# Kernel optimization log

Measured on AMD Instinct MI355X. Metric: run time of the kernel, lower is better.

Reference implementation:

```python
import jax, jax.numpy as jnp
import numpy as np

BN_EPS = 1e-5
EPS_GIN = 0.0  # pyg GINConv default eps

N_NODES = 50000
N_EDGES = 800000
D_IN = 128
D_OUT = 128


def setup_inputs() -> dict:
    key = jax.random.key(0)
    ks = jax.random.split(key, 6)
    x = jax.random.normal(ks[0], (N_NODES, D_IN), dtype=jnp.float32)
    edge_index = jax.random.randint(ks[1], (2, N_EDGES), 0, N_NODES, dtype=jnp.int32)
    # glorot-ish scale for the two Linear layers
    s1 = 1.0 / np.sqrt(D_IN)
    s2 = 1.0 / np.sqrt(D_OUT)
    W1 = jax.random.normal(ks[2], (D_IN, D_OUT), dtype=jnp.float32) * s1
    b1 = jnp.zeros((D_OUT,), dtype=jnp.float32)
    gamma = jnp.ones((D_OUT,), dtype=jnp.float32)
    beta = jnp.zeros((D_OUT,), dtype=jnp.float32)
    W2 = jax.random.normal(ks[3], (D_OUT, D_OUT), dtype=jnp.float32) * s2
    b2 = jnp.zeros((D_OUT,), dtype=jnp.float32)
    return {"x": x, "edge_index": edge_index, "W1": W1, "b1": b1,
            "gamma": gamma, "beta": beta, "W2": W2, "b2": b2}


def reference(x, edge_index, W1, b1, gamma, beta, W2, b2):
    n = x.shape[0]
    src, dst = edge_index[0], edge_index[1]  # source_to_target flow
    # scatter-add neighbor aggregation: agg[i] = sum_{(j->i)} x[j]
    agg = jax.ops.segment_sum(x[src], dst, num_segments=n)
    h = (1.0 + EPS_GIN) * x + agg  # GIN combine
    # Linear -> BatchNorm1d (training-mode batch stats, biased var) -> ReLU -> Linear
    h = h @ W1 + b1
    mean = jnp.mean(h, axis=0)
    var = jnp.var(h, axis=0)
    h = (h - mean) * jax.lax.rsqrt(var + BN_EPS) * gamma + beta
    h = jax.nn.relu(h)
    return h @ W2 + b2
```

## Files before the change

kernel.cpp:

```cpp
#include <hip/hip_runtime.h>
#include <hip/hip_bf16.h>

#define D 128
#define ELLW 64
#define BCAP 8192

typedef short bf16x8 __attribute__((ext_vector_type(8)));
typedef float f32x4 __attribute__((ext_vector_type(4)));

__device__ __forceinline__ ushort f32_to_bf16_rne(float f) {
    uint b = __float_as_uint(f);
    b += 0x7fffu + ((b >> 16) & 1u);
    return (ushort)(b >> 16);
}
__device__ __forceinline__ float bf16_bits_to_f32(ushort u) {
    return __uint_as_float(((uint)u) << 16);
}


__global__ __launch_bounds__(256) void prep_kernel(const float2* __restrict__ x2,
                                                   const float* __restrict__ W1,
                                                   const float* __restrict__ W2,
                                                   uint* __restrict__ xb,
                                                   ushort* __restrict__ W1T,
                                                   ushort* __restrict__ W2T,
                                                   int nhalf, int nbx) {
    int b = blockIdx.x, t = threadIdx.x;
    if (b < nbx) {
        int i = b * 256 + t;
        if (i < nhalf) {
            float2 v = x2[i];
            xb[i] = ((uint)f32_to_bf16_rne(v.y) << 16) | (uint)f32_to_bf16_rne(v.x);
        }
    } else {
        int wb = b - nbx;
        const float* W = (wb < 64) ? W1 : W2;
        ushort* WT = (wb < 64) ? W1T : W2T;
        int q = wb & 63;
        int nrow = q * 2 + (t >> 7);
        int k = t & 127;
        WT[nrow * D + k] = f32_to_bf16_rne(W[k * D + nrow]);
    }
}


__global__ __launch_bounds__(1024) void bucket_scatter_kernel(const int* __restrict__ src,
                                                              const int* __restrict__ dst,
                                                              uint* __restrict__ part,
                                                              int* __restrict__ bcnt, int m) {
    __shared__ int hist[256];
    __shared__ int cur[256];
    int t = threadIdx.x;
    if (t < 256) hist[t] = 0;
    __syncthreads();

    int base = blockIdx.x * 4096;
    uint v[4];
    int bk[4];
    bool ok[4];
#pragma unroll
    for (int j = 0; j < 4; ++j) {
        int e = base + j * 1024 + t;
        ok[j] = e < m;
        bk[j] = 0;
        if (ok[j]) {
            int s_ = src[e], d_ = dst[e];
            v[j] = ((uint)s_ << 16) | (uint)d_;
            bk[j] = d_ >> 8;
            atomicAdd(&hist[bk[j]], 1);
        }
    }
    __syncthreads();
    if (t < 256) {
        int h = hist[t];
        int g = h ? atomicAdd(&bcnt[t], h) : 0;
        cur[t] = t * BCAP + g;
    }
    __syncthreads();
#pragma unroll
    for (int j = 0; j < 4; ++j) {
        if (ok[j]) {
            int pos = atomicAdd(&cur[bk[j]], 1);
            if (pos - bk[j] * BCAP < BCAP)
                part[pos] = v[j];
        }
    }
}


__global__ __launch_bounds__(512) void bucket_ell_kernel(const uint* __restrict__ part,
                                                         const int* __restrict__ bcnt,
                                                         ushort* __restrict__ col_ell,
                                                         int* __restrict__ degv, int n) {
    __shared__ int lcur[256];
    int b = blockIdx.x, t = threadIdx.x;
    if (t < 256) lcur[t] = 0;
    __syncthreads();
    int cnt = min(bcnt[b], BCAP);
    const uint* pp = part + (size_t)b * BCAP;
    for (int i = t; i < cnt; i += 512) {
        uint v = pp[i];
        int node = (int)(v & 0xffffu);
        int r = node - (b << 8);
        int s = atomicAdd(&lcur[r], 1);
        s = min(s, ELLW - 1);
        col_ell[(size_t)node * ELLW + s] = (ushort)(v >> 16);
    }
    __syncthreads();
    int node0 = b << 8;
    if (t < 256 && node0 + t < n) degv[node0 + t] = lcur[t];
}


__global__ __launch_bounds__(256) void aggregate_kernel(const uint* __restrict__ xb,
                                                        const int* __restrict__ degv,
                                                        const ushort* __restrict__ col_ell,
                                                        uint* __restrict__ h0b, int n) {
    int node = blockIdx.x * 4 + (threadIdx.x >> 6);
    if (node >= n) return;
    int lane = threadIdx.x & 63;
    uint a = xb[node * 64 + lane];
    float sx = __uint_as_float(a << 16);
    float sy = __uint_as_float(a & 0xffff0000u);
    int deg = min(degv[node], ELLW);
    const ushort* lst = col_ell + (size_t)node * ELLW;
    int e = 0;
    for (; e + 3 < deg; e += 4) {
        int j0 = lst[e], j1 = lst[e + 1], j2 = lst[e + 2], j3 = lst[e + 3];
        uint u0 = xb[j0 * 64 + lane];
        uint u1 = xb[j1 * 64 + lane];
        uint u2 = xb[j2 * 64 + lane];
        uint u3 = xb[j3 * 64 + lane];
        sx += __uint_as_float(u0 << 16); sy += __uint_as_float(u0 & 0xffff0000u);
        sx += __uint_as_float(u1 << 16); sy += __uint_as_float(u1 & 0xffff0000u);
        sx += __uint_as_float(u2 << 16); sy += __uint_as_float(u2 & 0xffff0000u);
        sx += __uint_as_float(u3 << 16); sy += __uint_as_float(u3 & 0xffff0000u);
    }
    for (; e < deg; ++e) {
        uint u = xb[lst[e] * 64 + lane];
        sx += __uint_as_float(u << 16);
        sy += __uint_as_float(u & 0xffff0000u);
    }
    h0b[node * 64 + lane] = ((uint)f32_to_bf16_rne(sy) << 16) | (uint)f32_to_bf16_rne(sx);
}


template <bool BN_IN, bool STATS>
__global__ __launch_bounds__(256) void gemm_mfma_kernel(const ushort* __restrict__ inb,
                                                        const ushort* __restrict__ WT,
                                                        const float* __restrict__ bias,
                                                        void* __restrict__ outp,
                                                        const float* __restrict__ scale_shift,
                                                        float* __restrict__ bn_sums,
                                                        int N) {
    __shared__ __align__(16) ushort hs[64 * D];
    __shared__ __align__(16) ushort wt[D * D];
    __shared__ float ss[2 * D];
    __shared__ float bs[D];
    __shared__ float bnl[2 * D];

    int tid = threadIdx.x;
    int row0 = blockIdx.x * 64;
    if (tid < D) bs[tid] = bias[tid];
    if (BN_IN) ss[tid] = scale_shift[tid];
    if (STATS && tid < 2 * D) bnl[tid] = 0.f;
    __syncthreads();

    char* hsb = (char*)hs;
    char* wtb = (char*)wt;

#pragma unroll
    for (int it = 0; it < 8; ++it) {
        int c = it * 256 + tid;
        int wn = c >> 4, k8 = c & 15;
        bf16x8 v = *(const bf16x8*)(WT + wn * D + k8 * 8);
        *(bf16x8*)(wtb + wn * 256 + ((k8 * 16) ^ ((wn & 7) << 4))) = v;
    }
#pragma unroll
    for (int it = 0; it < 4; ++it) {
        int c = it * 256 + tid;
        int row = c >> 4, k8 = c & 15;
        int gr = row0 + row;
        bf16x8 v;
        if (gr < N) {
            v = *(const bf16x8*)(inb + (size_t)gr * D + k8 * 8);
        } else {
#pragma unroll
            for (int j = 0; j < 8; ++j) v[j] = 0;
        }
        if (BN_IN) {
#pragma unroll
            for (int j = 0; j < 8; ++j) {
                int k = k8 * 8 + j;
                float f = bf16_bits_to_f32((ushort)v[j]);
                f = fmaxf(f * ss[k] + ss[D + k], 0.f);
                v[j] = (short)f32_to_bf16_rne(f);
            }
        }
        *(bf16x8*)(hsb + row * 256 + ((k8 * 16) ^ ((row & 7) << 4))) = v;
    }
    __syncthreads();

    int w = tid >> 6, l = tid & 63;
    int lrow = l & 15, lk = l >> 4;

    f32x4 acc[8];
#pragma unroll
    for (int f = 0; f < 8; ++f) acc[f] = (f32x4){0.f, 0.f, 0.f, 0.f};

    bf16x8 afr[4];
    int arow = w * 16 + lrow;
#pragma unroll
    for (int t = 0; t < 4; ++t)
        afr[t] = *(const bf16x8*)(hsb + arow * 256 + ((t * 64 + lk * 16) ^ ((arow & 7) << 4)));

#pragma unroll
    for (int f = 0; f < 8; ++f) {
        int nc = f * 16 + lrow;
#pragma unroll
        for (int t = 0; t < 4; ++t) {
            bf16x8 bfr = *(const bf16x8*)(wtb + nc * 256 + ((t * 64 + lk * 16) ^ ((nc & 7) << 4)));
            acc[f] = __builtin_amdgcn_mfma_f32_16x16x32_bf16(afr[t], bfr, acc[f], 0, 0, 0);
        }
    }

    int rbase = row0 + w * 16 + lk * 4;
#pragma unroll
    for (int f = 0; f < 8; ++f) {
        int colc = f * 16 + lrow;
        float bv = bs[colc];
        float s = 0.f, q = 0.f;
#pragma unroll
        for (int r = 0; r < 4; ++r) {
            int gr = rbase + r;
            if (gr < N) {
                float v = acc[f][r] + bv;
                if (STATS) {
                    ((ushort*)outp)[(size_t)gr * D + colc] = f32_to_bf16_rne(v);
                    s += v;
                    q += v * v;
                } else {
                    ((float*)outp)[(size_t)gr * D + colc] = v;
                }
            }
        }
        if (STATS) {
            s += __shfl_xor(s, 16, 64);
            s += __shfl_xor(s, 32, 64);
            q += __shfl_xor(q, 16, 64);
            q += __shfl_xor(q, 32, 64);
            if (l < 16) {
                atomicAdd(&bnl[colc], s);
                atomicAdd(&bnl[D + colc], q);
            }
        }
    }
    if (STATS) {
        __syncthreads();
        if (tid < 2 * D) atomicAdd(&bn_sums[tid], bnl[tid]);
    }
}


__global__ __launch_bounds__(128) void bn_finalize_kernel(const float* __restrict__ bn_sums,
                                                          const float* __restrict__ gamma,
                                                          const float* __restrict__ beta,
                                                          float* __restrict__ scale_shift, float invn) {
    int c = threadIdx.x;
    float mean = bn_sums[c] * invn;
    float var = bn_sums[D + c] * invn - mean * mean;
    float rstd = rsqrtf(var + 1e-5f);
    float sc = gamma[c] * rstd;
    scale_shift[c] = sc;
    scale_shift[D + c] = beta[c] - mean * sc;
}


extern "C" void kernel_launch(void* const* d_in, const int* in_sizes, int n_in,
                              void* d_out, int out_size, void* d_ws, size_t ws_size,
                              hipStream_t stream) {
    const float* x = (const float*)d_in[0];
    const int* edge = (const int*)d_in[1];
    const float* W1 = (const float*)d_in[2];
    const float* b1 = (const float*)d_in[3];
    const float* gamma = (const float*)d_in[4];
    const float* beta = (const float*)d_in[5];
    const float* W2 = (const float*)d_in[6];
    const float* b2 = (const float*)d_in[7];

    int n = in_sizes[0] / D;
    int m = in_sizes[1] / 2;
    const int* src = edge;
    const int* dst = edge + m;

    int nbuck = (n + 255) >> 8;

    auto al = [](size_t o) { return (o + 63) & ~(size_t)63; };
    char* ws = (char*)d_ws;
    size_t off = 0;
    uint* xb = (uint*)(ws + off);
    ushort* h1b = (ushort*)(ws + off);
    off = al(off + (size_t)n * 64 * sizeof(uint));
    ushort* col_ell = (ushort*)(ws + off); off = al(off + (size_t)n * ELLW * sizeof(ushort));
    int* degv = (int*)(ws + off);     off = al(off + (size_t)n * sizeof(int));
    uint* part = (uint*)(ws + off);   off = al(off + (size_t)nbuck * BCAP * sizeof(uint));
    int* bcnt = (int*)(ws + off);     off += 256 * sizeof(int);
    float* bn_sums = (float*)(ws + off); off = al(off + 2 * D * sizeof(float));
    ushort* W1T = (ushort*)(ws + off); off = al(off + (size_t)D * D * sizeof(ushort));
    ushort* W2T = (ushort*)(ws + off); off = al(off + (size_t)D * D * sizeof(ushort));
    float* scale_shift = (float*)(ws + off); off = al(off + 2 * D * sizeof(float));

    uint* h0b = (uint*)d_out;

    int nbx = (n * 64 + 255) / 256;
    int nbs = (m + 4095) / 4096;

    hipMemsetAsync(bcnt, 0, 256 * sizeof(int) + 2 * D * sizeof(float), stream);
    prep_kernel<<<nbx + 128, 256, 0, stream>>>((const float2*)x, W1, W2, xb, W1T, W2T, n * 64, nbx);
    bucket_scatter_kernel<<<nbs, 1024, 0, stream>>>(src, dst, part, bcnt, m);
    bucket_ell_kernel<<<nbuck, 512, 0, stream>>>(part, bcnt, col_ell, degv, n);
    aggregate_kernel<<<(n + 3) / 4, 256, 0, stream>>>(xb, degv, col_ell, h0b, n);
    gemm_mfma_kernel<false, true><<<(n + 63) / 64, 256, 0, stream>>>((const ushort*)h0b, W1T, b1, h1b,
                                                                     nullptr, bn_sums, n);
    bn_finalize_kernel<<<1, 128, 0, stream>>>(bn_sums, gamma, beta, scale_shift, 1.0f / (float)n);
    gemm_mfma_kernel<true, false><<<(n + 63) / 64, 256, 0, stream>>>(h1b, W2T, b2, d_out,
                                                                     scale_shift, nullptr, n);
}
```

Measured before the change: 122.4 us.

## Fuse prep with bucket scatter, fold BN finalize into GEMM2, unroll gather

Merges the bf16 conversion/weight transpose kernel with the edge bucket scatter kernel into a single 1024-thread launch, and computes the BatchNorm scale/shift inside the second GEMM's prologue instead of a separate one-block kernel. This removes two kernel launches and their dependency gaps. The aggregate loop is widened to 8 independent gathers in flight per iteration. The price is per-block redundant recomputation of BN scale/shift and a heterogeneous mega-kernel with 1024-thread blocks, which can affect occupancy.

```diff
diff --git a/kernel.cpp b/kernel.cpp
--- a/kernel.cpp
+++ b/kernel.cpp
@@ -18,43 +18,42 @@
 }
 
 
-__global__ __launch_bounds__(256) void prep_kernel(const float2* __restrict__ x2,
-                                                   const float* __restrict__ W1,
-                                                   const float* __restrict__ W2,
-                                                   uint* __restrict__ xb,
-                                                   ushort* __restrict__ W1T,
-                                                   ushort* __restrict__ W2T,
-                                                   int nhalf, int nbx) {
+__global__ __launch_bounds__(1024) void prep_scatter_kernel(const float2* __restrict__ x2,
+                                                            const float* __restrict__ W1,
+                                                            const float* __restrict__ W2,
+                                                            const int* __restrict__ src,
+                                                            const int* __restrict__ dst,
+                                                            uint* __restrict__ xb,
+                                                            ushort* __restrict__ W1T,
+                                                            ushort* __restrict__ W2T,
+                                                            uint* __restrict__ part,
+                                                            int* __restrict__ bcnt,
+                                                            int nhalf, int m, int nbx) {
     int b = blockIdx.x, t = threadIdx.x;
     if (b < nbx) {
-        int i = b * 256 + t;
+        int i = b * 1024 + t;
         if (i < nhalf) {
             float2 v = x2[i];
             xb[i] = ((uint)f32_to_bf16_rne(v.y) << 16) | (uint)f32_to_bf16_rne(v.x);
         }
-    } else {
+        return;
+    }
+    if (b < nbx + 32) {
         int wb = b - nbx;
-        const float* W = (wb < 64) ? W1 : W2;
-        ushort* WT = (wb < 64) ? W1T : W2T;
-        int q = wb & 63;
-        int nrow = q * 2 + (t >> 7);
+        const float* W = (wb < 16) ? W1 : W2;
+        ushort* WT = (wb < 16) ? W1T : W2T;
+        int q = wb & 15;
+        int nrow = q * 8 + (t >> 7);
         int k = t & 127;
         WT[nrow * D + k] = f32_to_bf16_rne(W[k * D + nrow]);
-    }
-}
-
-
-__global__ __launch_bounds__(1024) void bucket_scatter_kernel(const int* __restrict__ src,
-                                                              const int* __restrict__ dst,
-                                                              uint* __restrict__ part,
-                                                              int* __restrict__ bcnt, int m) {
+        return;
+    }
     __shared__ int hist[256];
     __shared__ int cur[256];
-    int t = threadIdx.x;
     if (t < 256) hist[t] = 0;
     __syncthreads();
 
-    int base = blockIdx.x * 4096;
+    int base = (b - nbx - 32) * 4096;
     uint v[4];
     int bk[4];
     bool ok[4];
@@ -125,19 +124,29 @@
     int deg = min(degv[node], ELLW);
     const ushort* lst = col_ell + (size_t)node * ELLW;
     int e = 0;
-    for (; e + 3 < deg; e += 4) {
-        int j0 = lst[e], j1 = lst[e + 1], j2 = lst[e + 2], j3 = lst[e + 3];
-        uint u0 = xb[j0 * 64 + lane];
-        uint u1 = xb[j1 * 64 + lane];
-        uint u2 = xb[j2 * 64 + lane];
-        uint u3 = xb[j3 * 64 + lane];
-        sx += __uint_as_float(u0 << 16); sy += __uint_as_float(u0 & 0xffff0000u);
-        sx += __uint_as_float(u1 << 16); sy += __uint_as_float(u1 & 0xffff0000u);
-        sx += __uint_as_float(u2 << 16); sy += __uint_as_float(u2 & 0xffff0000u);
-        sx += __uint_as_float(u3 << 16); sy += __uint_as_float(u3 & 0xffff0000u);
+    for (; e + 7 < deg; e += 8) {
+        uint u[8];
+#pragma unroll
+        for (int j = 0; j < 8; ++j) u[j] = xb[(int)lst[e + j] * 64 + lane];
+#pragma unroll
+        for (int j = 0; j < 8; ++j) {
+            sx += __uint_as_float(u[j] << 16);
+            sy += __uint_as_float(u[j] & 0xffff0000u);
+        }
+    }
+    if (e + 3 < deg) {
+        uint u[4];
+#pragma unroll
+        for (int j = 0; j < 4; ++j) u[j] = xb[(int)lst[e + j] * 64 + lane];
+#pragma unroll
+        for (int j = 0; j < 4; ++j) {
+            sx += __uint_as_float(u[j] << 16);
+            sy += __uint_as_float(u[j] & 0xffff0000u);
+        }
+        e += 4;
     }
     for (; e < deg; ++e) {
-        uint u = xb[lst[e] * 64 + lane];
+        uint u = xb[(int)lst[e] * 64 + lane];
         sx += __uint_as_float(u << 16);
         sy += __uint_as_float(u & 0xffff0000u);
     }
@@ -150,9 +159,10 @@
                                                         const ushort* __restrict__ WT,
                                                         const float* __restrict__ bias,
                                                         void* __restrict__ outp,
-                                                        const float* __restrict__ scale_shift,
+                                                        const float* __restrict__ gamma,
+                                                        const float* __restrict__ beta,
                                                         float* __restrict__ bn_sums,
-                                                        int N) {
+                                                        float invn, int N) {
     __shared__ __align__(16) ushort hs[64 * D];
     __shared__ __align__(16) ushort wt[D * D];
     __shared__ float ss[2 * D];
@@ -162,7 +172,13 @@
     int tid = threadIdx.x;
     int row0 = blockIdx.x * 64;
     if (tid < D) bs[tid] = bias[tid];
-    if (BN_IN) ss[tid] = scale_shift[tid];
+    if (BN_IN && tid < D) {
+        float mean = bn_sums[tid] * invn;
+        float var = bn_sums[D + tid] * invn - mean * mean;
+        float sc = gamma[tid] * rsqrtf(var + 1e-5f);
+        ss[tid] = sc;
+        ss[D + tid] = beta[tid] - mean * sc;
+    }
     if (STATS && tid < 2 * D) bnl[tid] = 0.f;
     __syncthreads();
 
@@ -259,20 +275,6 @@
         __syncthreads();
         if (tid < 2 * D) atomicAdd(&bn_sums[tid], bnl[tid]);
     }
-}
-
-
-__global__ __launch_bounds__(128) void bn_finalize_kernel(const float* __restrict__ bn_sums,
-                                                          const float* __restrict__ gamma,
-                                                          const float* __restrict__ beta,
-                                                          float* __restrict__ scale_shift, float invn) {
-    int c = threadIdx.x;
-    float mean = bn_sums[c] * invn;
-    float var = bn_sums[D + c] * invn - mean * mean;
-    float rstd = rsqrtf(var + 1e-5f);
-    float sc = gamma[c] * rstd;
-    scale_shift[c] = sc;
-    scale_shift[D + c] = beta[c] - mean * sc;
 }
 
 
@@ -308,21 +310,20 @@
     float* bn_sums = (float*)(ws + off); off = al(off + 2 * D * sizeof(float));
     ushort* W1T = (ushort*)(ws + off); off = al(off + (size_t)D * D * sizeof(ushort));
     ushort* W2T = (ushort*)(ws + off); off = al(off + (size_t)D * D * sizeof(ushort));
-    float* scale_shift = (float*)(ws + off); off = al(off + 2 * D * sizeof(float));
 
     uint* h0b = (uint*)d_out;
 
-    int nbx = (n * 64 + 255) / 256;
+    int nbx = (n * 64 + 1023) / 1024;
     int nbs = (m + 4095) / 4096;
 
     hipMemsetAsync(bcnt, 0, 256 * sizeof(int) + 2 * D * sizeof(float), stream);
-    prep_kernel<<<nbx + 128, 256, 0, stream>>>((const float2*)x, W1, W2, xb, W1T, W2T, n * 64, nbx);
-    bucket_scatter_kernel<<<nbs, 1024, 0, stream>>>(src, dst, part, bcnt, m);
+    prep_scatter_kernel<<<nbx + 32 + nbs, 1024, 0, stream>>>((const float2*)x, W1, W2, src, dst,
+                                                             xb, W1T, W2T, part, bcnt, n * 64, m, nbx);
     bucket_ell_kernel<<<nbuck, 512, 0, stream>>>(part, bcnt, col_ell, degv, n);
     aggregate_kernel<<<(n + 3) / 4, 256, 0, stream>>>(xb, degv, col_ell, h0b, n);
     gemm_mfma_kernel<false, true><<<(n + 63) / 64, 256, 0, stream>>>((const ushort*)h0b, W1T, b1, h1b,
-                                                                     nullptr, bn_sums, n);
-    bn_finalize_kernel<<<1, 128, 0, stream>>>(bn_sums, gamma, beta, scale_shift, 1.0f / (float)n);
+                                                                     nullptr, nullptr, bn_sums, 0.f, n);
     gemm_mfma_kernel<true, false><<<(n + 63) / 64, 256, 0, stream>>>(h1b, W2T, b2, d_out,
-                                                                     scale_shift, nullptr, n);
-}
+                                                                     gamma, beta, bn_sums,
+                                                                     1.0f / (float)n, n);
+}
```

New measurement: 113.9 us. -7.0%, faster.
